# Kernel tuning notes

Hardware: AMD Instinct MI355X
Metric: run time of the kernel (lower is better)

Reference implementation:

```python
import jax, jax.numpy as jnp
import numpy as np

R, N, E, F, D, A = 3, 50000, 800000, 128, 128, 64
EPS = 1e-5


def setup_inputs() -> dict:
    key = jax.random.key(0)
    ks = jax.random.split(key, 8)
    s = 0.05
    feat = jax.random.normal(ks[0], (N, F), jnp.float32)
    src = jax.random.randint(ks[1], (R, E), 0, N)
    dst = jax.random.randint(ks[2], (R, E), 0, N)
    W0 = jax.random.normal(ks[3], (R, F, D), jnp.float32) * s
    b0 = jnp.zeros((R, D), jnp.float32)
    W1 = jax.random.normal(ks[4], (R, D, D), jnp.float32) * s
    b1 = jnp.zeros((R, D), jnp.float32)
    ln_g = jnp.ones((R, D), jnp.float32)   # per-relation MessageTransform LayerNorm (shared across its 2 layers)
    ln_b = jnp.zeros((R, D), jnp.float32)
    LN_g = jnp.ones((D,), jnp.float32)     # final PROVGEM layer_norm
    LN_b = jnp.zeros((D,), jnp.float32)
    Wa1 = jax.random.normal(ks[5], (R, D, A), jnp.float32) * s  # semantic attention proj
    Wa2 = jax.random.normal(ks[6], (R, A), jnp.float32) * s     # semantic attention score vec
    return dict(feat=feat, src=src, dst=dst, W0=W0, b0=b0, W1=W1, b1=b1,
                ln_g=ln_g, ln_b=ln_b, LN_g=LN_g, LN_b=LN_b, Wa1=Wa1, Wa2=Wa2)


def _ln(x, g, b):
    mu = jnp.mean(x, axis=-1, keepdims=True)
    var = jnp.mean(jnp.square(x - mu), axis=-1, keepdims=True)
    return (x - mu) * jax.lax.rsqrt(var + EPS) * g + b


def _mean_agg(feat, src_r, dst_r):
    # copy_u + mean: gather source feats along edges, segment-mean into dst nodes
    msg = feat[src_r]                                            # [E, F]
    ssum = jax.ops.segment_sum(msg, dst_r, num_segments=N)       # [N, F]
    deg = jax.ops.segment_sum(jnp.ones((E,), feat.dtype), dst_r, num_segments=N)
    return ssum / jnp.maximum(deg, 1.0)[:, None]                 # 0 for zero-degree nodes


def reference(feat, src, dst, W0, b0, W1, b1, ln_g, ln_b, LN_g, LN_b, Wa1, Wa2):
    # per-relation aggregation (loop over small fixed R=3)
    neigh = jnp.stack([_mean_agg(feat, src[r], dst[r]) for r in range(R)])  # [R, N, F]
    h = feat[None, :, :] + neigh                                            # residual add
    x = jnp.einsum('rnf,rfd->rnd', h, W0) + b0[:, None, :]
    x = jax.nn.relu(_ln(x, ln_g[:, None, :], ln_b[:, None, :]))
    x = jnp.einsum('rnd,rde->rne', x, W1) + b1[:, None, :]
    x = jax.nn.relu(_ln(x, ln_g[:, None, :], ln_b[:, None, :]))
    # final LayerNorm over [R, N, D]
    h = _ln(x, LN_g, LN_b)
    # semantic attention over relations
    e = jnp.einsum('rna,ra->rn', jnp.tanh(jnp.einsum('rnd,rda->rna', h, Wa1)), Wa2)
    attn = jax.nn.softmax(e, axis=0)                                        # softmax over relations
    return jnp.einsum('rn,rnd->nd', attn, h)                                # [N, D]
```

## Files before the change

### kernel.cpp

```cpp
#include <hip/hip_runtime.h>

#define RR 3
#define NN 50000
#define EE 800000
#define FF 128
#define DD 128
#define AA 64
#define EPSF 1e-5f
#define RN (RR * NN)
#define RE (RR * EE)
#define NTPR ((NN + 127) / 128)
#define NBK (RR * NTPR)
#define ECHUNK 8192
#define NEBLK ((RE + ECHUNK - 1) / ECHUNK)

typedef __attribute__((ext_vector_type(8))) short bf16x8;
typedef __attribute__((ext_vector_type(4))) float f32x4;

__device__ __forceinline__ short f2bs(float x) {
    union { float f; unsigned u; } v; v.f = x;
    unsigned rr = (v.u + 0x7fffu + ((v.u >> 16) & 1u)) >> 16;
    return (short)(rr & 0xffffu);
}

__device__ __forceinline__ float bs2f_lo(int p) {
    union { unsigned u; float f; } v; v.u = (unsigned)p << 16; return v.f;
}
__device__ __forceinline__ float bs2f_hi(int p) {
    union { unsigned u; float f; } v; v.u = (unsigned)p & 0xffff0000u; return v.f;
}

__device__ __forceinline__ int rel_of(long e) {
    return (e >= 2L * EE) ? 2 : ((e >= (long)EE) ? 1 : 0);
}

__global__ __launch_bounds__(256)
void feat2bf16(const float* __restrict__ feat, short* __restrict__ featb) {
    int gid = blockIdx.x * blockDim.x + threadIdx.x;
    if (gid >= NN * 16) return;
    f32x4 a = ((const f32x4*)feat)[2 * gid];
    f32x4 b = ((const f32x4*)feat)[2 * gid + 1];
    bf16x8 o;
    o[0] = f2bs(a.x); o[1] = f2bs(a.y); o[2] = f2bs(a.z); o[3] = f2bs(a.w);
    o[4] = f2bs(b.x); o[5] = f2bs(b.y); o[6] = f2bs(b.z); o[7] = f2bs(b.w);
    ((bf16x8*)featb)[gid] = o;
}

__global__ __launch_bounds__(256)
void count_kernel(const int* __restrict__ dst, int* __restrict__ cnt,
                  int* __restrict__ bcnt) {
    __shared__ int hist[NBK];
    for (int i = threadIdx.x; i < NBK; i += 256) hist[i] = 0;
    __syncthreads();
    long ebase = (long)blockIdx.x * ECHUNK;
    for (int i = threadIdx.x; i < ECHUNK; i += 256) {
        long e = ebase + i;
        if (e < RE) {
            int r = rel_of(e);
            int d = dst[e];
            atomicAdd(&cnt[r * NN + d], 1);
            atomicAdd(&hist[r * NTPR + (d >> 7)], 1);
        }
    }
    __syncthreads();
    for (int i = threadIdx.x; i < NBK; i += 256) {
        int v = hist[i];
        if (v) atomicAdd(&bcnt[i], v);
    }
}

__global__ __launch_bounds__(256)
void scan_phase1(const int* __restrict__ cnt, int* __restrict__ bsum) {
    __shared__ int sm[4];
    int b = blockIdx.x, t = threadIdx.x;
    int base = b * 1024 + t * 4;
    int s = 0;
    if (base + 3 < RN) {
        int4 v = *(const int4*)(cnt + base);
        s = v.x + v.y + v.z + v.w;
    } else {
        for (int i = 0; i < 4; ++i) if (base + i < RN) s += cnt[base + i];
    }
    #pragma unroll
    for (int m = 1; m < 64; m <<= 1) s += __shfl_xor(s, m);
    if ((t & 63) == 0) sm[t >> 6] = s;
    __syncthreads();
    if (t == 0) bsum[b] = sm[0] + sm[1] + sm[2] + sm[3];
}

__global__ __launch_bounds__(256)
void scan_phase2(int* __restrict__ bsum, int nb) {
    __shared__ int sm[256];
    int t = threadIdx.x;
    int v = (t < nb) ? bsum[t] : 0;
    sm[t] = v;
    __syncthreads();
    for (int d = 1; d < 256; d <<= 1) {
        int u = (t >= d) ? sm[t - d] : 0;
        __syncthreads();
        sm[t] += u;
        __syncthreads();
    }
    if (t < nb) bsum[t] = sm[t] - v;
}

__global__ __launch_bounds__(256)
void scan_phase3(const int* __restrict__ cnt, const int* __restrict__ bsum,
                 int* __restrict__ off) {
    __shared__ int sm[256];
    int b = blockIdx.x, t = threadIdx.x;
    int base = b * 1024 + t * 4;
    int c0 = 0, c1 = 0, c2 = 0, c3 = 0;
    if (base + 3 < RN) {
        int4 v = *(const int4*)(cnt + base);
        c0 = v.x; c1 = v.y; c2 = v.z; c3 = v.w;
    } else {
        if (base + 0 < RN) c0 = cnt[base + 0];
        if (base + 1 < RN) c1 = cnt[base + 1];
        if (base + 2 < RN) c2 = cnt[base + 2];
        if (base + 3 < RN) c3 = cnt[base + 3];
    }
    int s = c0 + c1 + c2 + c3;
    sm[t] = s;
    __syncthreads();
    for (int d = 1; d < 256; d <<= 1) {
        int u = (t >= d) ? sm[t - d] : 0;
        __syncthreads();
        sm[t] += u;
        __syncthreads();
    }
    int pre = bsum[b] + sm[t] - s;
    if (base + 0 < RN) off[base + 0] = pre;
    if (base + 1 < RN) off[base + 1] = pre + c0;
    if (base + 2 < RN) off[base + 2] = pre + c0 + c1;
    if (base + 3 < RN) off[base + 3] = pre + c0 + c1 + c2;
}

__global__ __launch_bounds__(256)
void bscan_kernel(const int* __restrict__ bcnt, int* __restrict__ bstart,
                  int* __restrict__ boff) {
    __shared__ int sm[256];
    int t = threadIdx.x;
    int loc[5];
    int s = 0;
    #pragma unroll
    for (int i = 0; i < 5; ++i) {
        int idx = t * 5 + i;
        int v = (idx < NBK) ? bcnt[idx] : 0;
        loc[i] = v; s += v;
    }
    sm[t] = s;
    __syncthreads();
    for (int d = 1; d < 256; d <<= 1) {
        int u = (t >= d) ? sm[t - d] : 0;
        __syncthreads();
        sm[t] += u;
        __syncthreads();
    }
    int run = sm[t] - s;
    #pragma unroll
    for (int i = 0; i < 5; ++i) {
        int idx = t * 5 + i;
        if (idx < NBK) { bstart[idx] = run; boff[idx] = run; run += loc[i]; }
    }
}

__global__ __launch_bounds__(256)
void bscatterA(const int* __restrict__ src, const int* __restrict__ dst,
               int* __restrict__ boff, unsigned* __restrict__ bpair) {
    __shared__ int hist[NBK];
    __shared__ int base[NBK];
    for (int i = threadIdx.x; i < NBK; i += 256) hist[i] = 0;
    __syncthreads();
    long ebase = (long)blockIdx.x * ECHUNK;
    for (int i = threadIdx.x; i < ECHUNK; i += 256) {
        long e = ebase + i;
        if (e < RE)
            atomicAdd(&hist[rel_of(e) * NTPR + (dst[e] >> 7)], 1);
    }
    __syncthreads();
    for (int i = threadIdx.x; i < NBK; i += 256) {
        int v = hist[i];
        base[i] = v ? atomicAdd(&boff[i], v) : 0;
    }
    __syncthreads();
    for (int i = threadIdx.x; i < ECHUNK; i += 256) {
        long e = ebase + i;
        if (e < RE) {
            int r = rel_of(e);
            int d = dst[e];
            int b = r * NTPR + (d >> 7);
            int pos = atomicAdd(&base[b], 1);
            bpair[pos] = ((unsigned)(d & 127) << 16) | (unsigned)src[e];
        }
    }
}

__global__ __launch_bounds__(256)
void scatterB(const unsigned* __restrict__ bpair, const int* __restrict__ bstart,
              const int* __restrict__ bcnt, const int* __restrict__ off,
              int* __restrict__ csr) {
    __shared__ int nb[128], cur[128];
    int b = blockIdx.x;
    int r = b / NTPR, tile = b - r * NTPR;
    if (threadIdx.x < 128) {
        int nloc = tile * 128 + threadIdx.x;
        nb[threadIdx.x] = (nloc < NN) ? off[r * NN + nloc] : 0;
        cur[threadIdx.x] = 0;
    }
    __syncthreads();
    int start = bstart[b], end = start + bcnt[b];
    for (int i = start + threadIdx.x; i < end; i += 256) {
        unsigned p = bpair[i];
        int d = (int)(p >> 16);
        int rank = atomicAdd(&cur[d], 1);
        csr[nb[d] + rank] = (int)(p & 0xFFFFu);
    }
}

__global__ __launch_bounds__(256)
void gather_kernel(const short* __restrict__ featb,
                   const int* __restrict__ csr,
                   const int* __restrict__ off,
                   const int* __restrict__ cnt,
                   short* __restrict__ ssumb) {
    int gid = blockIdx.x * blockDim.x + threadIdx.x;
    int w = gid >> 6, lane = gid & 63;
    if (w >= RN) return;
    int c = cnt[w];
    int start = off[w];
    int end = start + c;
    const int* f2 = (const int*)featb;
    float ax0 = 0.f, ay0 = 0.f, ax1 = 0.f, ay1 = 0.f;
    float ax2 = 0.f, ay2 = 0.f, ax3 = 0.f, ay3 = 0.f;
    int j = start;
    for (; j + 3 < end; j += 4) {
        int s0 = csr[j + 0];
        int s1 = csr[j + 1];
        int s2 = csr[j + 2];
        int s3 = csr[j + 3];
        int v0 = f2[(size_t)s0 * 64 + lane];
        int v1 = f2[(size_t)s1 * 64 + lane];
        int v2 = f2[(size_t)s2 * 64 + lane];
        int v3 = f2[(size_t)s3 * 64 + lane];
        ax0 += bs2f_lo(v0); ay0 += bs2f_hi(v0);
        ax1 += bs2f_lo(v1); ay1 += bs2f_hi(v1);
        ax2 += bs2f_lo(v2); ay2 += bs2f_hi(v2);
        ax3 += bs2f_lo(v3); ay3 += bs2f_hi(v3);
    }
    for (; j < end; ++j) {
        int s = csr[j];
        int v = f2[(size_t)s * 64 + lane];
        ax0 += bs2f_lo(v); ay0 += bs2f_hi(v);
    }
    float ax = (ax0 + ax1) + (ax2 + ax3);
    float ay = (ay0 + ay1) + (ay2 + ay3);
    float inv = 1.0f / fmaxf((float)c, 1.0f);
    int n = w % NN;
    int fv = f2[(size_t)n * 64 + lane];
    float hx = bs2f_lo(fv) + ax * inv;
    float hy = bs2f_hi(fv) + ay * inv;
    unsigned plo = (unsigned short)f2bs(hx);
    unsigned phi = (unsigned short)f2bs(hy);
    ((int*)ssumb)[(size_t)w * 64 + lane] = (int)((phi << 16) | plo);
}

#define TW 8

__device__ __forceinline__ void mfma_layer(const bf16x8 A[2][4], const short* Wlds,
                                           int g8, int c, f32x4 acc[2][8]) {
    #pragma unroll
    for (int kk = 0; kk < 4; ++kk) {
        #pragma unroll
        for (int t = 0; t < 8; ++t) {
            int d = t * 16 + c;
            bf16x8 B = *(const bf16x8*)&Wlds[d * 128 + ((kk * 32 + g8) ^ ((d & 7) << 3))];
            acc[0][t] = __builtin_amdgcn_mfma_f32_16x16x32_bf16(A[0][kk], B, acc[0][t], 0, 0, 0);
            acc[1][t] = __builtin_amdgcn_mfma_f32_16x16x32_bf16(A[1][kk], B, acc[1][t], 0, 0, 0);
        }
    }
}

template <bool RELU, bool BIAS>
__device__ __forceinline__ void ln_block(f32x4 acc[2][8], const float* bias,
                                         const float* gam, const float* bet, int c) {
    #pragma unroll
    for (int sub = 0; sub < 2; ++sub) {
        float s0 = 0, s1 = 0, s2 = 0, s3 = 0, p0 = 0, p1 = 0, p2 = 0, p3 = 0;
        #pragma unroll
        for (int t = 0; t < 8; ++t) {
            if (BIAS) {
                float bb = bias[t * 16 + c];
                acc[sub][t][0] += bb; acc[sub][t][1] += bb;
                acc[sub][t][2] += bb; acc[sub][t][3] += bb;
            }
            s0 += acc[sub][t][0]; p0 += acc[sub][t][0] * acc[sub][t][0];
            s1 += acc[sub][t][1]; p1 += acc[sub][t][1] * acc[sub][t][1];
            s2 += acc[sub][t][2]; p2 += acc[sub][t][2] * acc[sub][t][2];
            s3 += acc[sub][t][3]; p3 += acc[sub][t][3] * acc[sub][t][3];
        }
        #pragma unroll
        for (int m = 1; m < 16; m <<= 1) {
            s0 += __shfl_xor(s0, m); s1 += __shfl_xor(s1, m);
            s2 += __shfl_xor(s2, m); s3 += __shfl_xor(s3, m);
            p0 += __shfl_xor(p0, m); p1 += __shfl_xor(p1, m);
            p2 += __shfl_xor(p2, m); p3 += __shfl_xor(p3, m);
        }
        const float inv = 1.0f / 128.0f;
        float mu0 = s0 * inv, mu1 = s1 * inv, mu2 = s2 * inv, mu3 = s3 * inv;
        float r0 = rsqrtf(p0 * inv - mu0 * mu0 + EPSF);
        float r1 = rsqrtf(p1 * inv - mu1 * mu1 + EPSF);
        float r2 = rsqrtf(p2 * inv - mu2 * mu2 + EPSF);
        float r3 = rsqrtf(p3 * inv - mu3 * mu3 + EPSF);
        #pragma unroll
        for (int t = 0; t < 8; ++t) {
            float gg = gam[t * 16 + c], bb = bet[t * 16 + c];
            float v0 = (acc[sub][t][0] - mu0) * r0 * gg + bb;
            float v1 = (acc[sub][t][1] - mu1) * r1 * gg + bb;
            float v2 = (acc[sub][t][2] - mu2) * r2 * gg + bb;
            float v3 = (acc[sub][t][3] - mu3) * r3 * gg + bb;
            if (RELU) {
                v0 = fmaxf(v0, 0.f); v1 = fmaxf(v1, 0.f);
                v2 = fmaxf(v2, 0.f); v3 = fmaxf(v3, 0.f);
            }
            acc[sub][t][0] = v0; acc[sub][t][1] = v1;
            acc[sub][t][2] = v2; acc[sub][t][3] = v3;
        }
    }
}

__device__ __forceinline__ void store_ht(const f32x4 acc[2][8], short* myht, int g, int c) {
    #pragma unroll
    for (int sub = 0; sub < 2; ++sub)
        #pragma unroll
        for (int t = 0; t < 8; ++t) {
            int col = t * 16 + c;
            #pragma unroll
            for (int qq = 0; qq < 4; ++qq) {
                int row = sub * 16 + g * 4 + qq;
                myht[row * 128 + (col ^ ((row & 7) << 3))] = f2bs(acc[sub][t][qq]);
            }
        }
}

__device__ __forceinline__ void load_A(bf16x8 A[2][4], const short* myht, int g8, int c) {
    #pragma unroll
    for (int sub = 0; sub < 2; ++sub)
        #pragma unroll
        for (int kk = 0; kk < 4; ++kk) {
            int row = sub * 16 + c;
            A[sub][kk] = *(const bf16x8*)&myht[row * 128 + ((kk * 32 + g8) ^ ((row & 7) << 3))];
        }
}

__global__ __launch_bounds__(512)
void fused_transform(short* hbuf,
                     const float* __restrict__ W0, const float* __restrict__ b0,
                     const float* __restrict__ W1, const float* __restrict__ b1,
                     const float* __restrict__ ln_g, const float* __restrict__ ln_b,
                     const float* __restrict__ LN_g, const float* __restrict__ LN_b,
                     const float* __restrict__ Wa1, const float* __restrict__ Wa2,
                     float* __restrict__ evec) {
    __shared__ short W0t[FF * DD];
    __shared__ short W1t[DD * DD];
    __shared__ short Wa1t[AA * DD];
    __shared__ short ht[TW][32 * DD];
    __shared__ float b0s[DD], b1s[DD], lgs[DD], lbs[DD], Lgs[DD], Lbs[DD], wa2s[AA];

    const int r = blockIdx.y;
    const int tid = threadIdx.x;

    for (int i = tid; i < FF * DD; i += 512) {
        int k = i >> 7, d = i & 127;
        int idx = d * 128 + (k ^ ((d & 7) << 3));
        W0t[idx] = f2bs(W0[(size_t)r * FF * DD + i]);
        W1t[idx] = f2bs(W1[(size_t)r * DD * DD + i]);
    }
    for (int i = tid; i < DD * AA; i += 512) {
        int k = i >> 6, a = i & 63;
        Wa1t[a * 128 + (k ^ ((a & 7) << 3))] = f2bs(Wa1[(size_t)r * DD * AA + i]);
    }
    if (tid < DD) {
        b0s[tid] = b0[r * DD + tid];
        b1s[tid] = b1[r * DD + tid];
        lgs[tid] = ln_g[r * DD + tid];
        lbs[tid] = ln_b[r * DD + tid];
        Lgs[tid] = LN_g[tid];
        Lbs[tid] = LN_b[tid];
    }
    if (tid < AA) wa2s[tid] = Wa2[r * AA + tid];
    __syncthreads();

    const int wv = tid >> 6, ln = tid & 63;
    const int g = ln >> 4, c = ln & 15;
    const int g8 = g * 8;
    short* myht = ht[wv];

    const int ntiles = (NN + 31) / 32;
    for (int tile = blockIdx.x * TW + wv; tile < ntiles; tile += gridDim.x * TW) {
        const int nbase = tile * 32;

        bf16x8 A1[2][4];
        #pragma unroll
        for (int sub = 0; sub < 2; ++sub) {
            int n = nbase + sub * 16 + c;
            if (n > NN - 1) n = NN - 1;
            const short* sp = hbuf + ((size_t)r * NN + n) * FF;
            #pragma unroll
            for (int kk = 0; kk < 4; ++kk)
                A1[sub][kk] = *(const bf16x8*)(sp + kk * 32 + g8);
        }

        f32x4 acc[2][8];
        #pragma unroll
        for (int sub = 0; sub < 2; ++sub)
            #pragma unroll
            for (int t = 0; t < 8; ++t) acc[sub][t] = (f32x4){0.f, 0.f, 0.f, 0.f};

        mfma_layer(A1, W0t, g8, c, acc);
        ln_block<true, true>(acc, b0s, lgs, lbs, c);
        store_ht(acc, myht, g, c);

        bf16x8 A2[2][4];
        load_A(A2, myht, g8, c);
        #pragma unroll
        for (int sub = 0; sub < 2; ++sub)
            #pragma unroll
            for (int t = 0; t < 8; ++t) acc[sub][t] = (f32x4){0.f, 0.f, 0.f, 0.f};
        mfma_layer(A2, W1t, g8, c, acc);
        ln_block<true, true>(acc, b1s, lgs, lbs, c);
        ln_block<false, false>(acc, nullptr, Lgs, Lbs, c);
        store_ht(acc, myht, g, c);

        {
            short* gout = hbuf + ((size_t)r * NN + nbase) * FF;
            const int rows_valid = (nbase + 32 <= NN) ? 32 : (NN - nbase);
            #pragma unroll
            for (int cc = 0; cc < 8; ++cc) {
                int row = cc * 4 + (ln >> 4);
                int col0 = (ln & 15) * 8;
                bf16x8 v = *(const bf16x8*)&myht[row * 128 + (col0 ^ ((row & 7) << 3))];
                if (row < rows_valid) *(bf16x8*)&gout[row * FF + col0] = v;
            }
        }

        bf16x8 A3[2][4];
        load_A(A3, myht, g8, c);
        f32x4 accA[2][4];
        #pragma unroll
        for (int sub = 0; sub < 2; ++sub)
            #pragma unroll
            for (int t = 0; t < 4; ++t) accA[sub][t] = (f32x4){0.f, 0.f, 0.f, 0.f};
        #pragma unroll
        for (int kk = 0; kk < 4; ++kk)
            #pragma unroll
            for (int t = 0; t < 4; ++t) {
                int a_ = t * 16 + c;
                bf16x8 B = *(const bf16x8*)&Wa1t[a_ * 128 + ((kk * 32 + g8) ^ ((a_ & 7) << 3))];
                accA[0][t] = __builtin_amdgcn_mfma_f32_16x16x32_bf16(A3[0][kk], B, accA[0][t], 0, 0, 0);
                accA[1][t] = __builtin_amdgcn_mfma_f32_16x16x32_bf16(A3[1][kk], B, accA[1][t], 0, 0, 0);
            }
        #pragma unroll
        for (int sub = 0; sub < 2; ++sub) {
            float e0 = 0, e1 = 0, e2 = 0, e3 = 0;
            #pragma unroll
            for (int t = 0; t < 4; ++t) {
                float w2v = wa2s[t * 16 + c];
                e0 += tanhf(accA[sub][t][0]) * w2v;
                e1 += tanhf(accA[sub][t][1]) * w2v;
                e2 += tanhf(accA[sub][t][2]) * w2v;
                e3 += tanhf(accA[sub][t][3]) * w2v;
            }
            #pragma unroll
            for (int m = 1; m < 16; m <<= 1) {
                e0 += __shfl_xor(e0, m); e1 += __shfl_xor(e1, m);
                e2 += __shfl_xor(e2, m); e3 += __shfl_xor(e3, m);
            }
            int nb = nbase + sub * 16 + g * 4;
            if (c == 0 && nb + 0 < NN) evec[(size_t)r * NN + nb + 0] = e0;
            if (c == 1 && nb + 1 < NN) evec[(size_t)r * NN + nb + 1] = e1;
            if (c == 2 && nb + 2 < NN) evec[(size_t)r * NN + nb + 2] = e2;
            if (c == 3 && nb + 3 < NN) evec[(size_t)r * NN + nb + 3] = e3;
        }
    }
}

__global__ __launch_bounds__(256)
void combine_kernel(const short* __restrict__ hfb,
                    const float* __restrict__ evec,
                    float* __restrict__ out) {
    int gid = blockIdx.x * blockDim.x + threadIdx.x;
    if (gid >= NN * 64) return;
    int n = gid >> 6, j = gid & 63;
    float e0 = evec[n], e1 = evec[NN + n], e2 = evec[2 * NN + n];
    float m = fmaxf(e0, fmaxf(e1, e2));
    float w0 = __expf(e0 - m), w1 = __expf(e1 - m), w2 = __expf(e2 - m);
    float inv = 1.0f / (w0 + w1 + w2);
    w0 *= inv; w1 *= inv; w2 *= inv;
    const int* h0 = (const int*)hfb + (size_t)n * 64;
    const int* h1 = (const int*)hfb + ((size_t)NN + n) * 64;
    const int* h2 = (const int*)hfb + ((size_t)2 * NN + n) * 64;
    int a = h0[j], b = h1[j], d = h2[j];
    float2 o;
    o.x = w0 * bs2f_lo(a) + w1 * bs2f_lo(b) + w2 * bs2f_lo(d);
    o.y = w0 * bs2f_hi(a) + w1 * bs2f_hi(b) + w2 * bs2f_hi(d);
    ((float2*)out)[(size_t)n * 64 + j] = o;
}

extern "C" void kernel_launch(void* const* d_in, const int* in_sizes, int n_in,
                              void* d_out, int out_size, void* d_ws, size_t ws_size,
                              hipStream_t stream) {
    const float* feat = (const float*)d_in[0];
    const int*   src  = (const int*)d_in[1];
    const int*   dst  = (const int*)d_in[2];
    const float* W0   = (const float*)d_in[3];
    const float* b0   = (const float*)d_in[4];
    const float* W1   = (const float*)d_in[5];
    const float* b1   = (const float*)d_in[6];
    const float* ln_g = (const float*)d_in[7];
    const float* ln_b = (const float*)d_in[8];
    const float* LN_g = (const float*)d_in[9];
    const float* LN_b = (const float*)d_in[10];
    const float* Wa1  = (const float*)d_in[11];
    const float* Wa2  = (const float*)d_in[12];
    float* out = (float*)d_out;

    short*    ssumb  = (short*)d_ws;
    short*    featb  = ssumb + (size_t)RN * FF;
    int*      cnt    = (int*)(featb + (size_t)NN * FF);
    int*      off    = cnt + RN;
    int*      csr    = off + RN;
    float*    evec   = (float*)(csr + RE);
    int*      bsum   = (int*)(evec + RN);
    int*      bcnt   = bsum + 256;
    int*      bstart = bcnt + NBK;
    int*      boff   = bstart + NBK;
    unsigned* bpair  = (unsigned*)(boff + NBK);

    const int NB = (RN + 1023) / 1024;

    feat2bf16<<<(NN * 16 + 255) / 256, 256, 0, stream>>>(feat, featb);
    hipMemsetAsync(cnt, 0, (size_t)RN * sizeof(int), stream);
    hipMemsetAsync(bcnt, 0, (size_t)NBK * sizeof(int), stream);
    count_kernel<<<NEBLK, 256, 0, stream>>>(dst, cnt, bcnt);
    scan_phase1<<<NB, 256, 0, stream>>>(cnt, bsum);
    scan_phase2<<<1, 256, 0, stream>>>(bsum, NB);
    scan_phase3<<<NB, 256, 0, stream>>>(cnt, bsum, off);
    bscan_kernel<<<1, 256, 0, stream>>>(bcnt, bstart, boff);
    bscatterA<<<NEBLK, 256, 0, stream>>>(src, dst, boff, bpair);
    scatterB<<<NBK, 256, 0, stream>>>(bpair, bstart, bcnt, off, csr);
    gather_kernel<<<(RN * 64 + 255) / 256, 256, 0, stream>>>(featb, csr, off, cnt, ssumb);

    const int ntiles = (NN + 31) / 32;
    fused_transform<<<dim3((ntiles + TW - 1) / TW, RR), 512, 0, stream>>>(
        ssumb, W0, b0, W1, b1, ln_g, ln_b, LN_g, LN_b, Wa1, Wa2, evec);
    combine_kernel<<<(NN * 64 + 255) / 256, 256, 0, stream>>>(ssumb, evec, out);
}
```

Measured before the change: 366.2 us.

## Prepack weights into MFMA fragment layout in global memory, drop LDS weight staging

Result: slower. 767.2 us (+109.5%).

```diff
diff --git a/kernel.cpp b/kernel.cpp
--- a/kernel.cpp
+++ b/kernel.cpp
@@ -34,6 +34,11 @@
     return (e >= 2L * EE) ? 2 : ((e >= (long)EE) ? 1 : 0);
 }
 
+__device__ __forceinline__ float ftanh(float x) {
+    float a = __expf(2.0f * fabsf(x));
+    return copysignf(1.0f - 2.0f / (a + 1.0f), x);
+}
+
 __global__ __launch_bounds__(256)
 void feat2bf16(const float* __restrict__ feat, short* __restrict__ featb) {
     int gid = blockIdx.x * blockDim.x + threadIdx.x;
@@ -44,6 +49,47 @@
     o[0] = f2bs(a.x); o[1] = f2bs(a.y); o[2] = f2bs(a.z); o[3] = f2bs(a.w);
     o[4] = f2bs(b.x); o[5] = f2bs(b.y); o[6] = f2bs(b.z); o[7] = f2bs(b.w);
     ((bf16x8*)featb)[gid] = o;
+}
+
+__global__ __launch_bounds__(256)
+void prep_wfrag(const float* __restrict__ W0, const float* __restrict__ W1,
+                const float* __restrict__ Wa1,
+                short* __restrict__ Wf0, short* __restrict__ Wf1,
+                short* __restrict__ Wa1f) {
+    int gid = blockIdx.x * blockDim.x + threadIdx.x;
+    if (gid >= RR * 80 * 64) return;
+    int lane = gid & 63;
+    int grp  = (gid >> 6) % 80;
+    int r    = gid / (80 * 64);
+    int g = lane >> 4, c = lane & 15;
+    if (grp < 64) {
+        int m = grp >> 5;
+        int sg = grp & 31;
+        int t = sg >> 2, kk = sg & 3;
+        const float* Wsrc = (m ? W1 : W0) + (size_t)r * FF * DD;
+        short* o = (m ? Wf1 : Wf0) + (size_t)r * 16384 + ((size_t)sg * 64 + lane) * 8;
+        int d = t * 16 + c;
+        bf16x8 v;
+        #pragma unroll
+        for (int j = 0; j < 8; ++j) {
+            int k = kk * 32 + g * 8 + j;
+            v[j] = f2bs(Wsrc[(size_t)k * DD + d]);
+        }
+        *(bf16x8*)o = v;
+    } else {
+        int sg = grp - 64;
+        int t = sg >> 2, kk = sg & 3;
+        const float* Wsrc = Wa1 + (size_t)r * DD * AA;
+        short* o = Wa1f + (size_t)r * 8192 + ((size_t)sg * 64 + lane) * 8;
+        int a = t * 16 + c;
+        bf16x8 v;
+        #pragma unroll
+        for (int j = 0; j < 8; ++j) {
+            int k = kk * 32 + g * 8 + j;
+            v[j] = f2bs(Wsrc[(size_t)k * AA + a]);
+        }
+        *(bf16x8*)o = v;
+    }
 }
 
 __global__ __launch_bounds__(256)
@@ -267,14 +313,14 @@
 
 #define TW 8
 
-__device__ __forceinline__ void mfma_layer(const bf16x8 A[2][4], const short* Wlds,
-                                           int g8, int c, f32x4 acc[2][8]) {
+__device__ __forceinline__ void mfma_layer_g(const bf16x8 A[2][4],
+                                             const short* __restrict__ Wf,
+                                             int ln, f32x4 acc[2][8]) {
     #pragma unroll
     for (int kk = 0; kk < 4; ++kk) {
         #pragma unroll
         for (int t = 0; t < 8; ++t) {
-            int d = t * 16 + c;
-            bf16x8 B = *(const bf16x8*)&Wlds[d * 128 + ((kk * 32 + g8) ^ ((d & 7) << 3))];
+            bf16x8 B = *(const bf16x8*)&Wf[((size_t)((t * 4 + kk) * 64 + ln)) * 8];
             acc[0][t] = __builtin_amdgcn_mfma_f32_16x16x32_bf16(A[0][kk], B, acc[0][t], 0, 0, 0);
             acc[1][t] = __builtin_amdgcn_mfma_f32_16x16x32_bf16(A[1][kk], B, acc[1][t], 0, 0, 0);
         }
@@ -353,33 +399,21 @@
         }
 }
 
-__global__ __launch_bounds__(512)
+__global__ __launch_bounds__(512, 4)
 void fused_transform(short* hbuf,
-                     const float* __restrict__ W0, const float* __restrict__ b0,
-                     const float* __restrict__ W1, const float* __restrict__ b1,
+                     const float* __restrict__ b0, const float* __restrict__ b1,
                      const float* __restrict__ ln_g, const float* __restrict__ ln_b,
                      const float* __restrict__ LN_g, const float* __restrict__ LN_b,
-                     const float* __restrict__ Wa1, const float* __restrict__ Wa2,
+                     const float* __restrict__ Wa2,
+                     const short* __restrict__ Wf0, const short* __restrict__ Wf1,
+                     const short* __restrict__ Wa1f,
                      float* __restrict__ evec) {
-    __shared__ short W0t[FF * DD];
-    __shared__ short W1t[DD * DD];
-    __shared__ short Wa1t[AA * DD];
     __shared__ short ht[TW][32 * DD];
     __shared__ float b0s[DD], b1s[DD], lgs[DD], lbs[DD], Lgs[DD], Lbs[DD], wa2s[AA];
 
     const int r = blockIdx.y;
     const int tid = threadIdx.x;
 
-    for (int i = tid; i < FF * DD; i += 512) {
-        int k = i >> 7, d = i & 127;
-        int idx = d * 128 + (k ^ ((d & 7) << 3));
-        W0t[idx] = f2bs(W0[(size_t)r * FF * DD + i]);
-        W1t[idx] = f2bs(W1[(size_t)r * DD * DD + i]);
-    }
-    for (int i = tid; i < DD * AA; i += 512) {
-        int k = i >> 6, a = i & 63;
-        Wa1t[a * 128 + (k ^ ((a & 7) << 3))] = f2bs(Wa1[(size_t)r * DD * AA + i]);
-    }
     if (tid < DD) {
         b0s[tid] = b0[r * DD + tid];
         b1s[tid] = b1[r * DD + tid];
@@ -391,6 +425,10 @@
     if (tid < AA) wa2s[tid] = Wa2[r * AA + tid];
     __syncthreads();
 
+    const short* Wf0r  = Wf0  + (size_t)r * 16384;
+    const short* Wf1r  = Wf1  + (size_t)r * 16384;
+    const short* Wa1fr = Wa1f + (size_t)r * 8192;
+
     const int wv = tid >> 6, ln = tid & 63;
     const int g = ln >> 4, c = ln & 15;
     const int g8 = g * 8;
@@ -417,7 +455,7 @@
             #pragma unroll
             for (int t = 0; t < 8; ++t) acc[sub][t] = (f32x4){0.f, 0.f, 0.f, 0.f};
 
-        mfma_layer(A1, W0t, g8, c, acc);
+        mfma_layer_g(A1, Wf0r, ln, acc);
         ln_block<true, true>(acc, b0s, lgs, lbs, c);
         store_ht(acc, myht, g, c);
 
@@ -427,7 +465,7 @@
         for (int sub = 0; sub < 2; ++sub)
             #pragma unroll
             for (int t = 0; t < 8; ++t) acc[sub][t] = (f32x4){0.f, 0.f, 0.f, 0.f};
-        mfma_layer(A2, W1t, g8, c, acc);
+        mfma_layer_g(A2, Wf1r, ln, acc);
         ln_block<true, true>(acc, b1s, lgs, lbs, c);
         ln_block<false, false>(acc, nullptr, Lgs, Lbs, c);
         store_ht(acc, myht, g, c);
@@ -455,8 +493,7 @@
         for (int kk = 0; kk < 4; ++kk)
             #pragma unroll
             for (int t = 0; t < 4; ++t) {
-                int a_ = t * 16 + c;
-                bf16x8 B = *(const bf16x8*)&Wa1t[a_ * 128 + ((kk * 32 + g8) ^ ((a_ & 7) << 3))];
+                bf16x8 B = *(const bf16x8*)&Wa1fr[((size_t)((t * 4 + kk) * 64 + ln)) * 8];
                 accA[0][t] = __builtin_amdgcn_mfma_f32_16x16x32_bf16(A3[0][kk], B, accA[0][t], 0, 0, 0);
                 accA[1][t] = __builtin_amdgcn_mfma_f32_16x16x32_bf16(A3[1][kk], B, accA[1][t], 0, 0, 0);
             }
@@ -466,10 +503,10 @@
             #pragma unroll
             for (int t = 0; t < 4; ++t) {
                 float w2v = wa2s[t * 16 + c];
-                e0 += tanhf(accA[sub][t][0]) * w2v;
-                e1 += tanhf(accA[sub][t][1]) * w2v;
-                e2 += tanhf(accA[sub][t][2]) * w2v;
-                e3 += tanhf(accA[sub][t][3]) * w2v;
+                e0 += ftanh(accA[sub][t][0]) * w2v;
+                e1 += ftanh(accA[sub][t][1]) * w2v;
+                e2 += ftanh(accA[sub][t][2]) * w2v;
+                e3 += ftanh(accA[sub][t][3]) * w2v;
             }
             #pragma unroll
             for (int m = 1; m < 16; m <<= 1) {
@@ -536,9 +573,13 @@
     int*      bstart = bcnt + NBK;
     int*      boff   = bstart + NBK;
     unsigned* bpair  = (unsigned*)(boff + NBK);
+    short*    wf0    = (short*)(bpair + RE);
+    short*    wf1    = wf0 + (size_t)RR * 16384;
+    short*    wa1f   = wf1 + (size_t)RR * 16384;
 
     const int NB = (RN + 1023) / 1024;
 
+    prep_wfrag<<<60, 256, 0, stream>>>(W0, W1, Wa1, wf0, wf1, wa1f);
     feat2bf16<<<(NN * 16 + 255) / 256, 256, 0, stream>>>(feat, featb);
     hipMemsetAsync(cnt, 0, (size_t)RN * sizeof(int), stream);
     hipMemsetAsync(bcnt, 0, (size_t)NBK * sizeof(int), stream);
@@ -553,6 +594,6 @@
 
     const int ntiles = (NN + 31) / 32;
     fused_transform<<<dim3((ntiles + TW - 1) / TW, RR), 512, 0, stream>>>(
-        ssumb, W0, b0, W1, b1, ln_g, ln_b, LN_g, LN_b, Wa1, Wa2, evec);
+        ssumb, b0, b1, ln_g, ln_b, LN_g, LN_b, Wa2, wf0, wf1, wa1f, evec);
     combine_kernel<<<(NN * 64 + 255) / 256, 256, 0, stream>>>(ssumb, evec, out);
 }
```

## Use 16-row wave tiles, 1024-thread persistent blocks, and fast tanh in transform

Applied to the files above, without the earlier changes.

Result: slower. 480.2 us (+31.1%).

```diff
diff --git a/kernel.cpp b/kernel.cpp
--- a/kernel.cpp
+++ b/kernel.cpp
@@ -32,6 +32,11 @@
 
 __device__ __forceinline__ int rel_of(long e) {
     return (e >= 2L * EE) ? 2 : ((e >= (long)EE) ? 1 : 0);
+}
+
+__device__ __forceinline__ float ftanh(float x) {
+    float a = __expf(2.0f * fabsf(x));
+    return copysignf(1.0f - 2.0f / (a + 1.0f), x);
 }
 
 __global__ __launch_bounds__(256)
@@ -265,95 +270,85 @@
     ((int*)ssumb)[(size_t)w * 64 + lane] = (int)((phi << 16) | plo);
 }
 
-#define TW 8
-
-__device__ __forceinline__ void mfma_layer(const bf16x8 A[2][4], const short* Wlds,
-                                           int g8, int c, f32x4 acc[2][8]) {
+#define TW 16
+
+__device__ __forceinline__ void mfma_layer(const bf16x8 A[4], const short* Wlds,
+                                           int g8, int c, f32x4 acc[8]) {
     #pragma unroll
     for (int kk = 0; kk < 4; ++kk) {
         #pragma unroll
         for (int t = 0; t < 8; ++t) {
             int d = t * 16 + c;
             bf16x8 B = *(const bf16x8*)&Wlds[d * 128 + ((kk * 32 + g8) ^ ((d & 7) << 3))];
-            acc[0][t] = __builtin_amdgcn_mfma_f32_16x16x32_bf16(A[0][kk], B, acc[0][t], 0, 0, 0);
-            acc[1][t] = __builtin_amdgcn_mfma_f32_16x16x32_bf16(A[1][kk], B, acc[1][t], 0, 0, 0);
+            acc[t] = __builtin_amdgcn_mfma_f32_16x16x32_bf16(A[kk], B, acc[t], 0, 0, 0);
         }
     }
 }
 
 template <bool RELU, bool BIAS>
-__device__ __forceinline__ void ln_block(f32x4 acc[2][8], const float* bias,
+__device__ __forceinline__ void ln_block(f32x4 acc[8], const float* bias,
                                          const float* gam, const float* bet, int c) {
-    #pragma unroll
-    for (int sub = 0; sub < 2; ++sub) {
-        float s0 = 0, s1 = 0, s2 = 0, s3 = 0, p0 = 0, p1 = 0, p2 = 0, p3 = 0;
+    float s0 = 0, s1 = 0, s2 = 0, s3 = 0, p0 = 0, p1 = 0, p2 = 0, p3 = 0;
+    #pragma unroll
+    for (int t = 0; t < 8; ++t) {
+        if (BIAS) {
+            float bb = bias[t * 16 + c];
+            acc[t][0] += bb; acc[t][1] += bb;
+            acc[t][2] += bb; acc[t][3] += bb;
+        }
+        s0 += acc[t][0]; p0 += acc[t][0] * acc[t][0];
+        s1 += acc[t][1]; p1 += acc[t][1] * acc[t][1];
+        s2 += acc[t][2]; p2 += acc[t][2] * acc[t][2];
+        s3 += acc[t][3]; p3 += acc[t][3] * acc[t][3];
+    }
+    #pragma unroll
+    for (int m = 1; m < 16; m <<= 1) {
+        s0 += __shfl_xor(s0, m); s1 += __shfl_xor(s1, m);
+        s2 += __shfl_xor(s2, m); s3 += __shfl_xor(s3, m);
+        p0 += __shfl_xor(p0, m); p1 += __shfl_xor(p1, m);
+        p2 += __shfl_xor(p2, m); p3 += __shfl_xor(p3, m);
+    }
+    const float inv = 1.0f / 128.0f;
+    float mu0 = s0 * inv, mu1 = s1 * inv, mu2 = s2 * inv, mu3 = s3 * inv;
+    float r0 = rsqrtf(p0 * inv - mu0 * mu0 + EPSF);
+    float r1 = rsqrtf(p1 * inv - mu1 * mu1 + EPSF);
+    float r2 = rsqrtf(p2 * inv - mu2 * mu2 + EPSF);
+    float r3 = rsqrtf(p3 * inv - mu3 * mu3 + EPSF);
+    #pragma unroll
+    for (int t = 0; t < 8; ++t) {
+        float gg = gam[t * 16 + c], bb = bet[t * 16 + c];
+        float v0 = (acc[t][0] - mu0) * r0 * gg + bb;
+        float v1 = (acc[t][1] - mu1) * r1 * gg + bb;
+        float v2 = (acc[t][2] - mu2) * r2 * gg + bb;
+        float v3 = (acc[t][3] - mu3) * r3 * gg + bb;
+        if (RELU) {
+            v0 = fmaxf(v0, 0.f); v1 = fmaxf(v1, 0.f);
+            v2 = fmaxf(v2, 0.f); v3 = fmaxf(v3, 0.f);
+        }
+        acc[t][0] = v0; acc[t][1] = v1;
+        acc[t][2] = v2; acc[t][3] = v3;
+    }
+}
+
+__device__ __forceinline__ void store_ht(const f32x4 acc[8], short* myht, int g, int c) {
+    #pragma unroll
+    for (int t = 0; t < 8; ++t) {
+        int col = t * 16 + c;
         #pragma unroll
-        for (int t = 0; t < 8; ++t) {
-            if (BIAS) {
-                float bb = bias[t * 16 + c];
-                acc[sub][t][0] += bb; acc[sub][t][1] += bb;
-                acc[sub][t][2] += bb; acc[sub][t][3] += bb;
-            }
-            s0 += acc[sub][t][0]; p0 += acc[sub][t][0] * acc[sub][t][0];
-            s1 += acc[sub][t][1]; p1 += acc[sub][t][1] * acc[sub][t][1];
-            s2 += acc[sub][t][2]; p2 += acc[sub][t][2] * acc[sub][t][2];
-            s3 += acc[sub][t][3]; p3 += acc[sub][t][3] * acc[sub][t][3];
-        }
-        #pragma unroll
-        for (int m = 1; m < 16; m <<= 1) {
-            s0 += __shfl_xor(s0, m); s1 += __shfl_xor(s1, m);
-            s2 += __shfl_xor(s2, m); s3 += __shfl_xor(s3, m);
-            p0 += __shfl_xor(p0, m); p1 += __shfl_xor(p1, m);
-            p2 += __shfl_xor(p2, m); p3 += __shfl_xor(p3, m);
-        }
-        const float inv = 1.0f / 128.0f;
-        float mu0 = s0 * inv, mu1 = s1 * inv, mu2 = s2 * inv, mu3 = s3 * inv;
-        float r0 = rsqrtf(p0 * inv - mu0 * mu0 + EPSF);
-        float r1 = rsqrtf(p1 * inv - mu1 * mu1 + EPSF);
-        float r2 = rsqrtf(p2 * inv - mu2 * mu2 + EPSF);
-        float r3 = rsqrtf(p3 * inv - mu3 * mu3 + EPSF);
-        #pragma unroll
-        for (int t = 0; t < 8; ++t) {
-            float gg = gam[t * 16 + c], bb = bet[t * 16 + c];
-            float v0 = (acc[sub][t][0] - mu0) * r0 * gg + bb;
-            float v1 = (acc[sub][t][1] - mu1) * r1 * gg + bb;
-            float v2 = (acc[sub][t][2] - mu2) * r2 * gg + bb;
-            float v3 = (acc[sub][t][3] - mu3) * r3 * gg + bb;
-            if (RELU) {
-                v0 = fmaxf(v0, 0.f); v1 = fmaxf(v1, 0.f);
-                v2 = fmaxf(v2, 0.f); v3 = fmaxf(v3, 0.f);
-            }
-            acc[sub][t][0] = v0; acc[sub][t][1] = v1;
-            acc[sub][t][2] = v2; acc[sub][t][3] = v3;
-        }
-    }
-}
-
-__device__ __forceinline__ void store_ht(const f32x4 acc[2][8], short* myht, int g, int c) {
-    #pragma unroll
-    for (int sub = 0; sub < 2; ++sub)
-        #pragma unroll
-        for (int t = 0; t < 8; ++t) {
-            int col = t * 16 + c;
-            #pragma unroll
-            for (int qq = 0; qq < 4; ++qq) {
-                int row = sub * 16 + g * 4 + qq;
-                myht[row * 128 + (col ^ ((row & 7) << 3))] = f2bs(acc[sub][t][qq]);
-            }
-        }
-}
-
-__device__ __forceinline__ void load_A(bf16x8 A[2][4], const short* myht, int g8, int c) {
-    #pragma unroll
-    for (int sub = 0; sub < 2; ++sub)
-        #pragma unroll
-        for (int kk = 0; kk < 4; ++kk) {
-            int row = sub * 16 + c;
-            A[sub][kk] = *(const bf16x8*)&myht[row * 128 + ((kk * 32 + g8) ^ ((row & 7) << 3))];
-        }
-}
-
-__global__ __launch_bounds__(512)
+        for (int qq = 0; qq < 4; ++qq) {
+            int row = g * 4 + qq;
+            myht[row * 128 + (col ^ ((row & 7) << 3))] = f2bs(acc[t][qq]);
+        }
+    }
+}
+
+__device__ __forceinline__ void load_A(bf16x8 A[4], const short* myht, int g8, int c) {
+    #pragma unroll
+    for (int kk = 0; kk < 4; ++kk)
+        A[kk] = *(const bf16x8*)&myht[c * 128 + ((kk * 32 + g8) ^ ((c & 7) << 3))];
+}
+
+__global__ __launch_bounds__(1024)
 void fused_transform(short* hbuf,
                      const float* __restrict__ W0, const float* __restrict__ b0,
                      const float* __restrict__ W1, const float* __restrict__ b1,
@@ -364,19 +359,19 @@
     __shared__ short W0t[FF * DD];
     __shared__ short W1t[DD * DD];
     __shared__ short Wa1t[AA * DD];
-    __shared__ short ht[TW][32 * DD];
+    __shared__ short ht[TW][16 * DD];
     __shared__ float b0s[DD], b1s[DD], lgs[DD], lbs[DD], Lgs[DD], Lbs[DD], wa2s[AA];
 
     const int r = blockIdx.y;
     const int tid = threadIdx.x;
 
-    for (int i = tid; i < FF * DD; i += 512) {
+    for (int i = tid; i < FF * DD; i += 1024) {
         int k = i >> 7, d = i & 127;
         int idx = d * 128 + (k ^ ((d & 7) << 3));
         W0t[idx] = f2bs(W0[(size_t)r * FF * DD + i]);
         W1t[idx] = f2bs(W1[(size_t)r * DD * DD + i]);
     }
-    for (int i = tid; i < DD * AA; i += 512) {
+    for (int i = tid; i < DD * AA; i += 1024) {
         int k = i >> 6, a = i & 63;
         Wa1t[a * 128 + (k ^ ((a & 7) << 3))] = f2bs(Wa1[(size_t)r * DD * AA + i]);
     }
@@ -396,37 +391,30 @@
     const int g8 = g * 8;
     short* myht = ht[wv];
 
-    const int ntiles = (NN + 31) / 32;
+    const int ntiles = NN / 16;
     for (int tile = blockIdx.x * TW + wv; tile < ntiles; tile += gridDim.x * TW) {
-        const int nbase = tile * 32;
-
-        bf16x8 A1[2][4];
-        #pragma unroll
-        for (int sub = 0; sub < 2; ++sub) {
-            int n = nbase + sub * 16 + c;
-            if (n > NN - 1) n = NN - 1;
-            const short* sp = hbuf + ((size_t)r * NN + n) * FF;
+        const int nbase = tile * 16;
+
+        bf16x8 A1[4];
+        {
+            const short* sp = hbuf + ((size_t)r * NN + nbase + c) * FF;
             #pragma unroll
             for (int kk = 0; kk < 4; ++kk)
-                A1[sub][kk] = *(const bf16x8*)(sp + kk * 32 + g8);
-        }
-
-        f32x4 acc[2][8];
+                A1[kk] = *(const bf16x8*)(sp + kk * 32 + g8);
+        }
+
+        f32x4 acc[8];
         #pragma unroll
-        for (int sub = 0; sub < 2; ++sub)
-            #pragma unroll
-            for (int t = 0; t < 8; ++t) acc[sub][t] = (f32x4){0.f, 0.f, 0.f, 0.f};
+        for (int t = 0; t < 8; ++t) acc[t] = (f32x4){0.f, 0.f, 0.f, 0.f};
 
         mfma_layer(A1, W0t, g8, c, acc);
         ln_block<true, true>(acc, b0s, lgs, lbs, c);
         store_ht(acc, myht, g, c);
 
-        bf16x8 A2[2][4];
+        bf16x8 A2[4];
         load_A(A2, myht, g8, c);
         #pragma unroll
-        for (int sub = 0; sub < 2; ++sub)
-            #pragma unroll
-            for (int t = 0; t < 8; ++t) acc[sub][t] = (f32x4){0.f, 0.f, 0.f, 0.f};
+        for (int t = 0; t < 8; ++t) acc[t] = (f32x4){0.f, 0.f, 0.f, 0.f};
         mfma_layer(A2, W1t, g8, c, acc);
         ln_block<true, true>(acc, b1s, lgs, lbs, c);
         ln_block<false, false>(acc, nullptr, Lgs, Lbs, c);
@@ -434,53 +422,48 @@
 
         {
             short* gout = hbuf + ((size_t)r * NN + nbase) * FF;
-            const int rows_valid = (nbase + 32 <= NN) ? 32 : (NN - nbase);
             #pragma unroll
-            for (int cc = 0; cc < 8; ++cc) {
-                int row = cc * 4 + (ln >> 4);
-                int col0 = (ln & 15) * 8;
+            for (int cc = 0; cc < 4; ++cc) {
+                int row = cc * 4 + g;
+                int col0 = c * 8;
                 bf16x8 v = *(const bf16x8*)&myht[row * 128 + (col0 ^ ((row & 7) << 3))];
-                if (row < rows_valid) *(bf16x8*)&gout[row * FF + col0] = v;
+                *(bf16x8*)&gout[row * FF + col0] = v;
             }
         }
 
-        bf16x8 A3[2][4];
+        bf16x8 A3[4];
         load_A(A3, myht, g8, c);
-        f32x4 accA[2][4];
+        f32x4 accA[4];
         #pragma unroll
-        for (int sub = 0; sub < 2; ++sub)
-            #pragma unroll
-            for (int t = 0; t < 4; ++t) accA[sub][t] = (f32x4){0.f, 0.f, 0.f, 0.f};
+        for (int t = 0; t < 4; ++t) accA[t] = (f32x4){0.f, 0.f, 0.f, 0.f};
         #pragma unroll
         for (int kk = 0; kk < 4; ++kk)
             #pragma unroll
             for (int t = 0; t < 4; ++t) {
                 int a_ = t * 16 + c;
                 bf16x8 B = *(const bf16x8*)&Wa1t[a_ * 128 + ((kk * 32 + g8) ^ ((a_ & 7) << 3))];
-                accA[0][t] = __builtin_amdgcn_mfma_f32_16x16x32_bf16(A3[0][kk], B, accA[0][t], 0, 0, 0);
-                accA[1][t] = __builtin_amdgcn_mfma_f32_16x16x32_bf16(A3[1][kk], B, accA[1][t], 0, 0, 0);
+                accA[t] = __builtin_amdgcn_mfma_f32_16x16x32_bf16(A3[kk], B, accA[t], 0, 0, 0);
             }
-        #pragma unroll
-        for (int sub = 0; sub < 2; ++sub) {
+        {
             float e0 = 0, e1 = 0, e2 = 0, e3 = 0;
             #pragma unroll
             for (int t = 0; t < 4; ++t) {
                 float w2v = wa2s[t * 16 + c];
-                e0 += tanhf(accA[sub][t][0]) * w2v;
-                e1 += tanhf(accA[sub][t][1]) * w2v;
-                e2 += tanhf(accA[sub][t][2]) * w2v;
-                e3 += tanhf(accA[sub][t][3]) * w2v;
+                e0 += ftanh(accA[t][0]) * w2v;
+                e1 += ftanh(accA[t][1]) * w2v;
+                e2 += ftanh(accA[t][2]) * w2v;
+                e3 += ftanh(accA[t][3]) * w2v;
             }
             #pragma unroll
             for (int m = 1; m < 16; m <<= 1) {
                 e0 += __shfl_xor(e0, m); e1 += __shfl_xor(e1, m);
                 e2 += __shfl_xor(e2, m); e3 += __shfl_xor(e3, m);
             }
-            int nb = nbase + sub * 16 + g * 4;
-            if (c == 0 && nb + 0 < NN) evec[(size_t)r * NN + nb + 0] = e0;
-            if (c == 1 && nb + 1 < NN) evec[(size_t)r * NN + nb + 1] = e1;
-            if (c == 2 && nb + 2 < NN) evec[(size_t)r * NN + nb + 2] = e2;
-            if (c == 3 && nb + 3 < NN) evec[(size_t)r * NN + nb + 3] = e3;
+            int nb = nbase + g * 4;
+            if (c == 0) evec[(size_t)r * NN + nb + 0] = e0;
+            if (c == 1) evec[(size_t)r * NN + nb + 1] = e1;
+            if (c == 2) evec[(size_t)r * NN + nb + 2] = e2;
+            if (c == 3) evec[(size_t)r * NN + nb + 3] = e3;
         }
     }
 }
@@ -551,8 +534,7 @@
     scatterB<<<NBK, 256, 0, stream>>>(bpair, bstart, bcnt, off, csr);
     gather_kernel<<<(RN * 64 + 255) / 256, 256, 0, stream>>>(featb, csr, off, cnt, ssumb);
 
-    const int ntiles = (NN + 31) / 32;
-    fused_transform<<<dim3((ntiles + TW - 1) / TW, RR), 512, 0, stream>>>(
+    fused_transform<<<dim3(85, RR), 1024, 0, stream>>>(
         ssumb, W0, b0, W1, b1, ln_g, ln_b, LN_g, LN_b, Wa1, Wa2, evec);
     combine_kernel<<<(NN * 64 + 255) / 256, 256, 0, stream>>>(ssumb, evec, out);
 }
```
